# Kernel tuning notes

Hardware: AMD Instinct MI355X
Metric: run time of the kernel (lower is better)

Reference implementation:

```python
import jax, jax.numpy as jnp
import numpy as np

HEADS = 16
DIM_HEAD = 64
SCALE = DIM_HEAD ** -0.5


def setup_inputs() -> dict:
    key = jax.random.key(0)
    ks = jax.random.split(key, 6)
    B, Nq, Nkv, D = 2, 512, 4096, 1024
    inner = HEADS * DIM_HEAD  # 1024
    s = 1.0 / np.sqrt(D)
    return {
        "q": jax.random.normal(ks[0], (B, Nq, D), jnp.float32),
        "kv": jax.random.normal(ks[1], (B, Nkv, D), jnp.float32),
        "mask": jnp.ones((B, Nkv), dtype=bool),
        "Wq": jax.random.normal(ks[2], (D, inner), jnp.float32) * s,
        "Wkv": jax.random.normal(ks[3], (D, 2 * inner), jnp.float32) * s,
        "Wo": jax.random.normal(ks[4], (inner, D), jnp.float32) * (1.0 / np.sqrt(inner)),
        "bo": jnp.zeros((D,), jnp.float32),
    }


def reference(q, kv, mask, Wq, Wkv, Wo, bo):
    B, Nq, D = q.shape
    Nkv = kv.shape[1]
    h, dh = HEADS, DIM_HEAD
    # projections
    qh = (q @ Wq).reshape(B, Nq, h, dh).transpose(0, 2, 1, 3)        # (B,h,Nq,dh)
    kvp = kv @ Wkv                                                    # (B,Nkv,2*inner)
    k, v = jnp.split(kvp, 2, axis=-1)
    kh = k.reshape(B, Nkv, h, dh).transpose(0, 2, 1, 3)              # (B,h,Nkv,dh)
    vh = v.reshape(B, Nkv, h, dh).transpose(0, 2, 1, 3)
    # scaled dot-product cross-attention
    attn = jnp.einsum("bhqd,bhkd->bhqk", qh, kh) * SCALE             # (B,h,Nq,Nkv)
    neg_inf = jnp.finfo(attn.dtype).min
    attn = jnp.where(mask[:, None, None, :], attn, neg_inf)
    attn = jax.nn.softmax(attn, axis=-1)
    out = jnp.einsum("bhqk,bhkd->bhqd", attn, vh)                    # (B,h,Nq,dh)
    out = out.transpose(0, 2, 1, 3).reshape(B, Nq, h * dh)
    return out @ Wo + bo
```

## Files before the change

### kernel.cpp

```cpp
#include <hip/hip_runtime.h>
#include <string.h>
#include <math.h>

typedef unsigned short u16;
typedef __bf16 bf16x8 __attribute__((ext_vector_type(8)));
typedef float floatx4 __attribute__((ext_vector_type(4)));

#define HEADS  16
#define DH     64
#define BATCH  2
#define NQ     512
#define NKV    4096
#define DMODEL 1024
#define INNER  1024
#define SCALE  0.125f
#define LOG2E  1.4426950408889634f
#define FM     12.0f
#define SPLIT  4
#define KEYS_PER_PART (NKV / SPLIT)
#define CH (KEYS_PER_PART / 64)

__device__ __forceinline__ u16 f2bf(float f) {
  union { __bf16 h; u16 u; } v; v.h = (__bf16)f; return v.u;
}

__device__ __forceinline__ void gll16(const u16* g, u16* l) {
  __builtin_amdgcn_global_load_lds(
      (const __attribute__((address_space(1))) unsigned int*)g,
      (__attribute__((address_space(3))) unsigned int*)l, 16, 0, 0);
}

__global__ __launch_bounds__(256) void prep(const float* __restrict__ q,
                                            const float* __restrict__ kv,
                                            const float* __restrict__ Wq,
                                            const float* __restrict__ Wkv,
                                            const float* __restrict__ Wo,
                                            u16* __restrict__ qb,
                                            u16* __restrict__ kvb,
                                            u16* __restrict__ Wqt,
                                            u16* __restrict__ Wkvt,
                                            u16* __restrict__ Wot) {
  __shared__ float tile[32][33];
  const int bx = blockIdx.x, tid = threadIdx.x;
  if (bx < 4608) {
    const float* x; u16* y; size_t i;
    if (bx < 512) { x = q;  y = qb;  i = (size_t)bx * 256 + tid; }
    else          { x = kv; y = kvb; i = (size_t)(bx - 512) * 256 + tid; }
    const float4* p = (const float4*)x + i * 2;
    float4 a = p[0], b = p[1];
    union { u16 s[8]; uint4 v; } o;
    o.s[0] = f2bf(a.x); o.s[1] = f2bf(a.y); o.s[2] = f2bf(a.z); o.s[3] = f2bf(a.w);
    o.s[4] = f2bf(b.x); o.s[5] = f2bf(b.y); o.s[6] = f2bf(b.z); o.s[7] = f2bf(b.w);
    *(uint4*)(y + i * 8) = o.v;
    return;
  }
  const float* W; u16* Wt; int K, N, n0, k0, t;
  if (bx < 5632)      { t = bx - 4608; W = Wq;  Wt = Wqt;  K = 1024; N = 1024; n0 = (t & 31) * 32; k0 = (t >> 5) * 32; }
  else if (bx < 7680) { t = bx - 5632; W = Wkv; Wt = Wkvt; K = 1024; N = 2048; n0 = (t & 63) * 32; k0 = (t >> 6) * 32; }
  else                { t = bx - 7680; W = Wo;  Wt = Wot;  K = 1024; N = 1024; n0 = (t & 31) * 32; k0 = (t >> 5) * 32; }
  const int tx = tid & 31, ty = tid >> 5;
  for (int i = 0; i < 32; i += 8)
    tile[ty + i][tx] = W[(size_t)(k0 + ty + i) * N + n0 + tx];
  __syncthreads();
  for (int i = 0; i < 32; i += 8)
    Wt[(size_t)(n0 + ty + i) * K + k0 + tx] = f2bf(tile[tx][ty + i]);
}

#define KV_NT 16
__global__ __launch_bounds__(256) void gemm_kv(const u16* __restrict__ A,
                                               const u16* __restrict__ Bt,
                                               u16* __restrict__ Kb,
                                               u16* __restrict__ vT) {
  const int K = DMODEL;
  __shared__ __align__(16) u16 As[2][128 * 64];
  __shared__ __align__(16) u16 Bs[2][128 * 64];
  const int tid  = threadIdx.x;
  const int lane = tid & 63, wave = tid >> 6;
  const int wr = wave >> 1, wc = wave & 1;
  const int l16 = lane & 15, quad = lane >> 4;
  const int d = blockIdx.x;
  const int lg = (d & 7) * 128 + (d >> 3);
  const int bm = lg >> 4, bn = lg & 15;
  const int r8 = lane >> 3;
  const int kb8 = (lane & 7) ^ r8;
  const u16* aP = A  + ((size_t)bm * 128 + wave * 8 + r8) * K + kb8 * 8;
  const u16* bP = Bt + ((size_t)bn * 128 + wave * 8 + r8) * K + kb8 * 8;

  floatx4 acc[4][4] = {};

#define KV_STAGE(t_) { \
    const int j_ = (t_) & 1; \
    const size_t ko = (size_t)(t_) * 64; \
    _Pragma("unroll") \
    for (int p = 0; p < 4; ++p) { \
      gll16(aP + (size_t)p * 32 * K + ko, &As[j_][p * 2048 + wave * 512]); \
      gll16(bP + (size_t)p * 32 * K + ko, &Bs[j_][p * 2048 + wave * 512]); \
    } \
  }

  KV_STAGE(0);
  asm volatile("s_waitcnt vmcnt(0)" ::: "memory");
  __builtin_amdgcn_s_barrier();

  for (int t = 0; t < KV_NT; ++t) {
    if (t + 1 < KV_NT) KV_STAGE(t + 1);
    const u16* Ab = As[t & 1];
    const u16* Bb = Bs[t & 1];
    bf16x8 af[4][2], bfr[4][2];
#pragma unroll
    for (int i = 0; i < 4; ++i)
#pragma unroll
      for (int h2 = 0; h2 < 2; ++h2)
        af[i][h2] = *(const bf16x8*)&Ab[(wr * 64 + i * 16 + l16) * 64 +
                                        (((h2 * 4 + quad) ^ (l16 & 7)) << 3)];
#pragma unroll
    for (int j = 0; j < 4; ++j)
#pragma unroll
      for (int h2 = 0; h2 < 2; ++h2)
        bfr[j][h2] = *(const bf16x8*)&Bb[(wc * 64 + j * 16 + l16) * 64 +
                                         (((h2 * 4 + quad) ^ (l16 & 7)) << 3)];
    __builtin_amdgcn_s_setprio(1);
#pragma unroll
    for (int i = 0; i < 4; ++i)
#pragma unroll
      for (int j = 0; j < 4; ++j) {
        acc[i][j] = __builtin_amdgcn_mfma_f32_16x16x32_bf16(af[i][0], bfr[j][0], acc[i][j], 0, 0, 0);
        acc[i][j] = __builtin_amdgcn_mfma_f32_16x16x32_bf16(af[i][1], bfr[j][1], acc[i][j], 0, 0, 0);
      }
    __builtin_amdgcn_s_setprio(0);
    asm volatile("s_waitcnt vmcnt(0)" ::: "memory");
    __builtin_amdgcn_s_barrier();
  }

  if (bn < 8) {
#pragma unroll
    for (int i = 0; i < 4; ++i) {
      const int rowb = bm * 128 + wr * 64 + i * 16 + quad * 4;
#pragma unroll
      for (int j = 0; j < 4; ++j) {
        const int col = bn * 128 + wc * 64 + j * 16 + l16;
#pragma unroll
        for (int r = 0; r < 4; ++r)
          Kb[(size_t)(rowb + r) * 1024 + col] = f2bf(acc[i][j][r]);
      }
    }
  } else {
    const int b = bm >> 5;
    const int tokb = (bm & 31) * 128;
#pragma unroll
    for (int i = 0; i < 4; ++i) {
      const int tok0 = tokb + wr * 64 + i * 16 + quad * 4;
#pragma unroll
      for (int j = 0; j < 4; ++j) {
        const int dd = (bn - 8) * 128 + wc * 64 + j * 16 + l16;
        union { u16 s[4]; uint2 v; } pk;
#pragma unroll
        for (int r = 0; r < 4; ++r) pk.s[r] = f2bf(acc[i][j][r]);
        *(uint2*)(vT + ((size_t)(b * 1024 + dd)) * NKV + tok0) = pk.v;
      }
    }
  }
#undef KV_STAGE
}

template<bool OUT_BF16>
__global__ __launch_bounds__(256) void gemm64(const u16* __restrict__ A,
                                              const u16* __restrict__ Bt,
                                              float* __restrict__ Cf,
                                              u16* __restrict__ Cb,
                                              const float* __restrict__ bias,
                                              int M, int N, int K) {
  __shared__ __align__(16) u16 As[2][64 * 64];
  __shared__ __align__(16) u16 Bs[2][64 * 64];
  const int tid = threadIdx.x;
  const int lane = tid & 63, wave = tid >> 6;
  const int wr = wave >> 1, wc = wave & 1;
  const int l16 = lane & 15, quad = lane >> 4;
  const int bm = blockIdx.y, bn = blockIdx.x;
  const int r0 = tid >> 3;
  const int kbs = (tid & 7) ^ (r0 & 7);
  const u16* aP0 = A  + ((size_t)bm * 64 + r0)      * K + kbs * 8;
  const u16* aP1 = A  + ((size_t)bm * 64 + r0 + 32) * K + kbs * 8;
  const u16* bP0 = Bt + ((size_t)bn * 64 + r0)      * K + kbs * 8;
  const u16* bP1 = Bt + ((size_t)bn * 64 + r0 + 32) * K + kbs * 8;

  floatx4 acc[2][2] = {};
  const int nt = K >> 6;

#define G64_STAGE(t_) { \
    const int j_ = (t_) & 1; \
    const size_t ko = (size_t)(t_) * 64; \
    gll16(aP0 + ko, &As[j_][wave * 512]); \
    gll16(aP1 + ko, &As[j_][2048 + wave * 512]); \
    gll16(bP0 + ko, &Bs[j_][wave * 512]); \
    gll16(bP1 + ko, &Bs[j_][2048 + wave * 512]); \
  }

  G64_STAGE(0);
  asm volatile("s_waitcnt vmcnt(0)" ::: "memory");
  __builtin_amdgcn_s_barrier();

  for (int t = 0; t < nt; ++t) {
    if (t + 1 < nt) G64_STAGE(t + 1);
    const u16* Ab = As[t & 1];
    const u16* Bb = Bs[t & 1];
    bf16x8 af[2][2], bfr[2][2];
#pragma unroll
    for (int i = 0; i < 2; ++i)
#pragma unroll
      for (int kk = 0; kk < 2; ++kk)
        af[i][kk] = *(const bf16x8*)&Ab[(wr * 32 + i * 16 + l16) * 64 +
                                        (((kk * 4 + quad) ^ (l16 & 7)) << 3)];
#pragma unroll
    for (int j = 0; j < 2; ++j)
#pragma unroll
      for (int kk = 0; kk < 2; ++kk)
        bfr[j][kk] = *(const bf16x8*)&Bs[t & 1][(wc * 32 + j * 16 + l16) * 64 +
                                               (((kk * 4 + quad) ^ (l16 & 7)) << 3)];
    __builtin_amdgcn_s_setprio(1);
#pragma unroll
    for (int i = 0; i < 2; ++i)
#pragma unroll
      for (int j = 0; j < 2; ++j) {
        acc[i][j] = __builtin_amdgcn_mfma_f32_16x16x32_bf16(af[i][0], bfr[j][0], acc[i][j], 0, 0, 0);
        acc[i][j] = __builtin_amdgcn_mfma_f32_16x16x32_bf16(af[i][1], bfr[j][1], acc[i][j], 0, 0, 0);
      }
    __builtin_amdgcn_s_setprio(0);
    asm volatile("s_waitcnt vmcnt(0)" ::: "memory");
    __builtin_amdgcn_s_barrier();
    (void)Bb;
  }
#undef G64_STAGE
#pragma unroll
  for (int i = 0; i < 2; ++i) {
    const int rowb = bm * 64 + wr * 32 + i * 16 + quad * 4;
#pragma unroll
    for (int j = 0; j < 2; ++j) {
      const int col = bn * 64 + wc * 32 + j * 16 + l16;
#pragma unroll
      for (int r = 0; r < 4; ++r) {
        const size_t idx = (size_t)(rowb + r) * N + col;
        if (OUT_BF16) Cb[idx] = f2bf(acc[i][j][r]);
        else          Cf[idx] = acc[i][j][r] + bias[col];
      }
    }
  }
}

__global__ __launch_bounds__(256) void attn_part(const u16* __restrict__ Qh,
                                                 const u16* __restrict__ Kb,
                                                 const u16* __restrict__ vT,
                                                 const int* __restrict__ mask,
                                                 float* __restrict__ Opart,
                                                 float* __restrict__ Mst,
                                                 float* __restrict__ Lst) {
  __shared__ __align__(16) u16 Ks[64 * 64];
  __shared__ __align__(16) u16 Vs[2][64 * 64];
  __shared__ __align__(16) u16 QP[4608];
  __shared__ float Msk[64];
  const int tid = threadIdx.x;
  const int lane = tid & 63, w = tid >> 6;
  const int l16 = lane & 15, quad = lane >> 4;
  const int d_ = blockIdx.x;
  const int lg = (d_ & 7) * 128 + (d_ >> 3);
  const int qt   = lg & 7;
  const int part = (lg >> 3) & 3;
  const int h    = (lg >> 5) & 15;
  const int b    = lg >> 9;
  const int rs = tid >> 2, d0 = (tid & 3) * 16;
  u16* Ps = QP + w * 1152;

  const int r8 = lane >> 3;
  const int kb8 = (lane & 7) ^ (r8 & 7);
  const int key00 = part * KEYS_PER_PART;
  const u16* kSrc = Kb + ((size_t)(b * NKV + key00 + w * 8 + r8)) * 1024 + h * DH + kb8 * 8;
  const u16* vSrc = vT + ((size_t)((b * 16 + h) * 64 + w * 8 + r8)) * NKV + key00 + kb8 * 8;
  u16* ldsK0 = Ks + w * 512;
  u16* ldsK1 = Ks + 2048 + w * 512;
  const int koA = (quad ^ (l16 & 7)) << 3;
  const int koB = ((quad + 4) ^ (l16 & 7)) << 3;

  bf16x8 bones;
  {
    union { u16 s[8]; bf16x8 v; } t1;
    const u16 o1 = (l16 == 0) ? (u16)0x3F80 : (u16)0;
#pragma unroll
    for (int i = 0; i < 8; ++i) t1.s[i] = o1;
    bones = t1.v;
  }

  {
    const uint4* p = (const uint4*)(Qh + ((size_t)(b * NQ + qt * 64 + rs)) * INNER + h * DH + d0);
    *(uint4*)&QP[rs * 72 + d0]     = p[0];
    *(uint4*)&QP[rs * 72 + d0 + 8] = p[1];
  }
  gll16(kSrc, ldsK0);
  gll16(kSrc + 32768, ldsK1);
  gll16(vSrc, Vs[0] + w * 512);
  gll16(vSrc + (size_t)32 * NKV, Vs[0] + 2048 + w * 512);
  float mk0 = 0.f;
  if (tid < 64) mk0 = (mask[(size_t)b * NKV + key00 + tid] != 0) ? -FM : -1e30f;
  __syncthreads();
  bf16x8 aq0 = *(const bf16x8*)&QP[(w * 16 + l16) * 72 + quad * 8];
  bf16x8 aq1 = *(const bf16x8*)&QP[(w * 16 + l16) * 72 + 32 + quad * 8];
  if (tid < 64) Msk[tid] = mk0;
  __syncthreads();

  floatx4 o[4] = {};
  floatx4 lacc = {0.f, 0.f, 0.f, 0.f};
  const float SC = SCALE * LOG2E;

  for (int c = 0; c < CH; ++c) {
    const u16* Vcur = Vs[c & 1];
#pragma unroll
    for (int nt = 0; nt < 4; ++nt) {
      bf16x8 b0 = *(const bf16x8*)&Ks[(nt * 16 + l16) * 64 + koA];
      bf16x8 b1 = *(const bf16x8*)&Ks[(nt * 16 + l16) * 64 + koB];
      floatx4 t = {0.f, 0.f, 0.f, 0.f};
      t = __builtin_amdgcn_mfma_f32_16x16x32_bf16(aq0, b0, t, 0, 0, 0);
      t = __builtin_amdgcn_mfma_f32_16x16x32_bf16(aq1, b1, t, 0, 0, 0);
      const float mk = Msk[nt * 16 + l16];
#pragma unroll
      for (int r = 0; r < 4; ++r)
        Ps[(quad * 4 + r) * 72 + nt * 16 + l16] = f2bf(exp2f(t[r] * SC + mk));
    }
    __syncthreads();
    if (c + 1 < CH) {
      gll16(kSrc + (size_t)(c + 1) * 65536, ldsK0);
      gll16(kSrc + (size_t)(c + 1) * 65536 + 32768, ldsK1);
      u16* vdst = Vs[(c + 1) & 1];
      gll16(vSrc + (c + 1) * 64, vdst + w * 512);
      gll16(vSrc + (c + 1) * 64 + (size_t)32 * NKV, vdst + 2048 + w * 512);
      if (tid < 64)
        Msk[tid] = (mask[(size_t)b * NKV + key00 + (c + 1) * 64 + tid] != 0) ? -FM : -1e30f;
    }
    bf16x8 ap0 = *(const bf16x8*)&Ps[l16 * 72 + quad * 8];
    bf16x8 ap1 = *(const bf16x8*)&Ps[l16 * 72 + 32 + quad * 8];
    lacc = __builtin_amdgcn_mfma_f32_16x16x32_bf16(ap0, bones, lacc, 0, 0, 0);
    lacc = __builtin_amdgcn_mfma_f32_16x16x32_bf16(ap1, bones, lacc, 0, 0, 0);
#pragma unroll
    for (int dt = 0; dt < 4; ++dt) {
      bf16x8 bv0 = *(const bf16x8*)&Vcur[(dt * 16 + l16) * 64 + koA];
      bf16x8 bv1 = *(const bf16x8*)&Vcur[(dt * 16 + l16) * 64 + koB];
      o[dt] = __builtin_amdgcn_mfma_f32_16x16x32_bf16(ap0, bv0, o[dt], 0, 0, 0);
      o[dt] = __builtin_amdgcn_mfma_f32_16x16x32_bf16(ap1, bv1, o[dt], 0, 0, 0);
    }
    __syncthreads();
  }
  const int pid = (((b * 16 + h) * 8 + qt) * 4) + part;
#pragma unroll
  for (int r = 0; r < 4; ++r) {
    const int q = w * 16 + quad * 4 + r;
    if (l16 == 0) { Mst[pid * 64 + q] = FM; Lst[pid * 64 + q] = lacc[r]; }
#pragma unroll
    for (int dt = 0; dt < 4; ++dt)
      Opart[(size_t)pid * 4096 + q * 64 + dt * 16 + l16] = o[dt][r];
  }
}

__global__ __launch_bounds__(256) void attn_combine(const float* __restrict__ Opart,
                                                    const float* __restrict__ Mst,
                                                    const float* __restrict__ Lst,
                                                    u16* __restrict__ Out) {
  const int x = blockIdx.x;
  const int t = threadIdx.x;
  const int q = t >> 2, db = (t & 3) * 16;
  const int b = x >> 7, h = (x >> 3) & 15, qt = x & 7;
  float ms[SPLIT], ls[SPLIT];
#pragma unroll
  for (int s = 0; s < SPLIT; ++s) {
    ms[s] = Mst[(size_t)(x * SPLIT + s) * 64 + q];
    ls[s] = Lst[(size_t)(x * SPLIT + s) * 64 + q];
  }
  float M = fmaxf(fmaxf(ms[0], ms[1]), fmaxf(ms[2], ms[3]));
  float wgt[SPLIT], L = 0.f;
#pragma unroll
  for (int s = 0; s < SPLIT; ++s) { wgt[s] = exp2f(ms[s] - M); L += wgt[s] * ls[s]; }
  const float inv = 1.0f / L;
  float acc[16] = {};
#pragma unroll
  for (int s = 0; s < SPLIT; ++s) {
    const float4* p = (const float4*)&Opart[(size_t)(x * SPLIT + s) * 4096 + q * 64 + db];
    const float ws = wgt[s];
#pragma unroll
    for (int i = 0; i < 4; ++i) {
      float4 v = p[i];
      acc[i * 4 + 0] += ws * v.x; acc[i * 4 + 1] += ws * v.y;
      acc[i * 4 + 2] += ws * v.z; acc[i * 4 + 3] += ws * v.w;
    }
  }
  union { u16 s[16]; uint4 v[2]; } ou;
#pragma unroll
  for (int i = 0; i < 16; ++i) ou.s[i] = f2bf(acc[i] * inv);
  u16* dst = Out + ((size_t)(b * NQ + qt * 64 + q)) * INNER + h * DH + db;
  *(uint4*)dst = ou.v[0]; *(uint4*)(dst + 8) = ou.v[1];
}

extern "C" void kernel_launch(void* const* d_in, const int* in_sizes, int n_in,
                              void* d_out, int out_size, void* d_ws, size_t ws_size,
                              hipStream_t stream) {
  const float* q    = (const float*)d_in[0];
  const float* kv   = (const float*)d_in[1];
  const int*   mask = (const int*)d_in[2];
  const float* Wq   = (const float*)d_in[3];
  const float* Wkv  = (const float*)d_in[4];
  const float* Wo   = (const float*)d_in[5];
  const float* bo   = (const float*)d_in[6];
  float* out = (float*)d_out;

  char* ws = (char*)d_ws;
  u16*   qb    = (u16*)(ws);
  u16*   kvb   = (u16*)(ws + (2u << 20));
  float* Mst   = (float*)(ws);
  float* Lst   = (float*)(ws + (256u << 10));
  float* Opart = (float*)(ws + (2u << 20));
  u16* Wqt  = (u16*)(ws + (18u << 20));
  u16* Wkvt = (u16*)(ws + (20u << 20));
  u16* Wot  = (u16*)(ws + (24u << 20));
  u16* qh   = (u16*)(ws + (26u << 20));
  u16* Kb   = (u16*)(ws + (28u << 20));
  u16* vT   = (u16*)(ws + (44u << 20));
  u16* attn = (u16*)(ws + (60u << 20));

  prep<<<dim3(8704), 256, 0, stream>>>(q, kv, Wq, Wkv, Wo, qb, kvb, Wqt, Wkvt, Wot);
  gemm64<true><<<dim3(INNER / 64, (BATCH * NQ) / 64), 256, 0, stream>>>(
      qb, Wqt, nullptr, qh, nullptr, BATCH * NQ, INNER, DMODEL);
  gemm_kv<<<dim3(1024), 256, 0, stream>>>(kvb, Wkvt, Kb, vT);
  attn_part<<<dim3(BATCH * HEADS * (NQ / 64) * SPLIT), 256, 0, stream>>>(
      qh, Kb, vT, mask, Opart, Mst, Lst);
  attn_combine<<<dim3(BATCH * HEADS * (NQ / 64)), 256, 0, stream>>>(Opart, Mst, Lst, attn);
  gemm64<false><<<dim3(DMODEL / 64, (BATCH * NQ) / 64), 256, 0, stream>>>(
      attn, Wot, out, nullptr, bo, BATCH * NQ, DMODEL, INNER);
}
```

Before: 215.6 us.

## Enlarge KV projection GEMM tiles to 256x256 with interleaved prefetch

The K/V projection GEMM now uses 256x256 output tiles with 8 waves per block (each wave computing 128x64) instead of 128x128 tiles with 4 waves. Prefetch of the next k-slice is split into four pieces interleaved between MFMA groups, so global-to-LDS loads overlap compute. The aim is less global traffic per FLOP and better latency hiding. The cost is 128 KB of LDS per block, a grid of only 256 blocks on a 256-CU part (roughly one wave per CU), and higher register pressure from the 32 accumulator tiles.

```diff
diff --git a/kernel.cpp b/kernel.cpp
--- a/kernel.cpp
+++ b/kernel.cpp
@@ -67,100 +67,139 @@
 }
 
 #define KV_NT 16
-__global__ __launch_bounds__(256) void gemm_kv(const u16* __restrict__ A,
-                                               const u16* __restrict__ Bt,
-                                               u16* __restrict__ Kb,
-                                               u16* __restrict__ vT) {
+__global__ __launch_bounds__(512, 2) void gemm_kv(const u16* __restrict__ A,
+                                                  const u16* __restrict__ Bt,
+                                                  u16* __restrict__ Kb,
+                                                  u16* __restrict__ vT) {
   const int K = DMODEL;
-  __shared__ __align__(16) u16 As[2][128 * 64];
-  __shared__ __align__(16) u16 Bs[2][128 * 64];
+  __shared__ __align__(16) u16 As[2][256 * 64];
+  __shared__ __align__(16) u16 Bs[2][256 * 64];
   const int tid  = threadIdx.x;
   const int lane = tid & 63, wave = tid >> 6;
-  const int wr = wave >> 1, wc = wave & 1;
+  const int wr = wave >> 2, wc = wave & 3;
   const int l16 = lane & 15, quad = lane >> 4;
   const int d = blockIdx.x;
-  const int lg = (d & 7) * 128 + (d >> 3);
-  const int bm = lg >> 4, bn = lg & 15;
+  const int lg = (d & 7) * 32 + (d >> 3);
+  const int bm = lg >> 3, bn = lg & 7;
   const int r8 = lane >> 3;
   const int kb8 = (lane & 7) ^ r8;
-  const u16* aP = A  + ((size_t)bm * 128 + wave * 8 + r8) * K + kb8 * 8;
-  const u16* bP = Bt + ((size_t)bn * 128 + wave * 8 + r8) * K + kb8 * 8;
-
-  floatx4 acc[4][4] = {};
-
-#define KV_STAGE(t_) { \
+  const u16* aP = A  + ((size_t)(bm * 256 + wave * 8 + r8)) * K + kb8 * 8;
+  const u16* bP = Bt + ((size_t)(bn * 256 + wave * 8 + r8)) * K + kb8 * 8;
+
+  floatx4 acc[8][4] = {};
+
+#define KV_STAGE_A(t_, h_) { \
     const int j_ = (t_) & 1; \
     const size_t ko = (size_t)(t_) * 64; \
-    _Pragma("unroll") \
-    for (int p = 0; p < 4; ++p) { \
-      gll16(aP + (size_t)p * 32 * K + ko, &As[j_][p * 2048 + wave * 512]); \
-      gll16(bP + (size_t)p * 32 * K + ko, &Bs[j_][p * 2048 + wave * 512]); \
-    } \
-  }
-
-  KV_STAGE(0);
-  asm volatile("s_waitcnt vmcnt(0)" ::: "memory");
-  __builtin_amdgcn_s_barrier();
+    gll16(aP + (size_t)((h_) * 128) * K + ko,      &As[j_][((h_) * 128) * 64 + wave * 512]); \
+    gll16(aP + (size_t)((h_) * 128 + 64) * K + ko, &As[j_][((h_) * 128 + 64) * 64 + wave * 512]); \
+  }
+#define KV_STAGE_B(t_, h_) { \
+    const int j_ = (t_) & 1; \
+    const size_t ko = (size_t)(t_) * 64; \
+    gll16(bP + (size_t)((h_) * 128) * K + ko,      &Bs[j_][((h_) * 128) * 64 + wave * 512]); \
+    gll16(bP + (size_t)((h_) * 128 + 64) * K + ko, &Bs[j_][((h_) * 128 + 64) * 64 + wave * 512]); \
+  }
+
+  KV_STAGE_A(0, 0); KV_STAGE_A(0, 1); KV_STAGE_B(0, 0); KV_STAGE_B(0, 1);
 
   for (int t = 0; t < KV_NT; ++t) {
-    if (t + 1 < KV_NT) KV_STAGE(t + 1);
+    asm volatile("s_waitcnt vmcnt(0)" ::: "memory");
+    __builtin_amdgcn_s_barrier();
     const u16* Ab = As[t & 1];
     const u16* Bb = Bs[t & 1];
-    bf16x8 af[4][2], bfr[4][2];
-#pragma unroll
-    for (int i = 0; i < 4; ++i)
+    const bool pf = (t + 1 < KV_NT);
+    bf16x8 bB[4][2], bA[4][2];
+    if (pf) KV_STAGE_A(t + 1, 0);
+#pragma unroll
+    for (int n = 0; n < 4; ++n)
 #pragma unroll
       for (int h2 = 0; h2 < 2; ++h2)
-        af[i][h2] = *(const bf16x8*)&Ab[(wr * 64 + i * 16 + l16) * 64 +
+        bB[n][h2] = *(const bf16x8*)&Bb[(wc * 64 + n * 16 + l16) * 64 +
                                         (((h2 * 4 + quad) ^ (l16 & 7)) << 3)];
 #pragma unroll
-    for (int j = 0; j < 4; ++j)
+    for (int i = 0; i < 4; ++i)
 #pragma unroll
       for (int h2 = 0; h2 < 2; ++h2)
-        bfr[j][h2] = *(const bf16x8*)&Bb[(wc * 64 + j * 16 + l16) * 64 +
-                                         (((h2 * 4 + quad) ^ (l16 & 7)) << 3)];
+        bA[i][h2] = *(const bf16x8*)&Ab[(wr * 128 + i * 16 + l16) * 64 +
+                                        (((h2 * 4 + quad) ^ (l16 & 7)) << 3)];
     __builtin_amdgcn_s_setprio(1);
 #pragma unroll
     for (int i = 0; i < 4; ++i)
 #pragma unroll
-      for (int j = 0; j < 4; ++j) {
-        acc[i][j] = __builtin_amdgcn_mfma_f32_16x16x32_bf16(af[i][0], bfr[j][0], acc[i][j], 0, 0, 0);
-        acc[i][j] = __builtin_amdgcn_mfma_f32_16x16x32_bf16(af[i][1], bfr[j][1], acc[i][j], 0, 0, 0);
+      for (int j = 0; j < 2; ++j) {
+        acc[i][j] = __builtin_amdgcn_mfma_f32_16x16x32_bf16(bA[i][0], bB[j][0], acc[i][j], 0, 0, 0);
+        acc[i][j] = __builtin_amdgcn_mfma_f32_16x16x32_bf16(bA[i][1], bB[j][1], acc[i][j], 0, 0, 0);
       }
     __builtin_amdgcn_s_setprio(0);
-    asm volatile("s_waitcnt vmcnt(0)" ::: "memory");
-    __builtin_amdgcn_s_barrier();
-  }
-
-  if (bn < 8) {
-#pragma unroll
-    for (int i = 0; i < 4; ++i) {
-      const int rowb = bm * 128 + wr * 64 + i * 16 + quad * 4;
-#pragma unroll
-      for (int j = 0; j < 4; ++j) {
-        const int col = bn * 128 + wc * 64 + j * 16 + l16;
+    if (pf) KV_STAGE_A(t + 1, 1);
+    __builtin_amdgcn_s_setprio(1);
+#pragma unroll
+    for (int i = 0; i < 4; ++i)
+#pragma unroll
+      for (int j = 2; j < 4; ++j) {
+        acc[i][j] = __builtin_amdgcn_mfma_f32_16x16x32_bf16(bA[i][0], bB[j][0], acc[i][j], 0, 0, 0);
+        acc[i][j] = __builtin_amdgcn_mfma_f32_16x16x32_bf16(bA[i][1], bB[j][1], acc[i][j], 0, 0, 0);
+      }
+    __builtin_amdgcn_s_setprio(0);
+    if (pf) KV_STAGE_B(t + 1, 0);
+#pragma unroll
+    for (int i = 0; i < 4; ++i)
+#pragma unroll
+      for (int h2 = 0; h2 < 2; ++h2)
+        bA[i][h2] = *(const bf16x8*)&Ab[(wr * 128 + 64 + i * 16 + l16) * 64 +
+                                        (((h2 * 4 + quad) ^ (l16 & 7)) << 3)];
+    __builtin_amdgcn_s_setprio(1);
+#pragma unroll
+    for (int i = 0; i < 4; ++i)
+#pragma unroll
+      for (int j = 0; j < 2; ++j) {
+        acc[4 + i][j] = __builtin_amdgcn_mfma_f32_16x16x32_bf16(bA[i][0], bB[j][0], acc[4 + i][j], 0, 0, 0);
+        acc[4 + i][j] = __builtin_amdgcn_mfma_f32_16x16x32_bf16(bA[i][1], bB[j][1], acc[4 + i][j], 0, 0, 0);
+      }
+    __builtin_amdgcn_s_setprio(0);
+    if (pf) KV_STAGE_B(t + 1, 1);
+    __builtin_amdgcn_s_setprio(1);
+#pragma unroll
+    for (int i = 0; i < 4; ++i)
+#pragma unroll
+      for (int j = 2; j < 4; ++j) {
+        acc[4 + i][j] = __builtin_amdgcn_mfma_f32_16x16x32_bf16(bA[i][0], bB[j][0], acc[4 + i][j], 0, 0, 0);
+        acc[4 + i][j] = __builtin_amdgcn_mfma_f32_16x16x32_bf16(bA[i][1], bB[j][1], acc[4 + i][j], 0, 0, 0);
+      }
+    __builtin_amdgcn_s_setprio(0);
+  }
+#undef KV_STAGE_A
+#undef KV_STAGE_B
+
+  if (bn < 4) {
+#pragma unroll
+    for (int m = 0; m < 8; ++m) {
+      const int rowb = bm * 256 + wr * 128 + m * 16 + quad * 4;
+#pragma unroll
+      for (int n = 0; n < 4; ++n) {
+        const int col = bn * 256 + wc * 64 + n * 16 + l16;
 #pragma unroll
         for (int r = 0; r < 4; ++r)
-          Kb[(size_t)(rowb + r) * 1024 + col] = f2bf(acc[i][j][r]);
+          Kb[(size_t)(rowb + r) * 1024 + col] = f2bf(acc[m][n][r]);
       }
     }
   } else {
-    const int b = bm >> 5;
-    const int tokb = (bm & 31) * 128;
-#pragma unroll
-    for (int i = 0; i < 4; ++i) {
-      const int tok0 = tokb + wr * 64 + i * 16 + quad * 4;
-#pragma unroll
-      for (int j = 0; j < 4; ++j) {
-        const int dd = (bn - 8) * 128 + wc * 64 + j * 16 + l16;
+#pragma unroll
+    for (int m = 0; m < 8; ++m) {
+      const int rowb = bm * 256 + wr * 128 + m * 16 + quad * 4;
+      const int b = rowb >> 12;
+      const int tok0 = rowb & 4095;
+#pragma unroll
+      for (int n = 0; n < 4; ++n) {
+        const int dd = (bn - 4) * 256 + wc * 64 + n * 16 + l16;
         union { u16 s[4]; uint2 v; } pk;
 #pragma unroll
-        for (int r = 0; r < 4; ++r) pk.s[r] = f2bf(acc[i][j][r]);
+        for (int r = 0; r < 4; ++r) pk.s[r] = f2bf(acc[m][n][r]);
         *(uint2*)(vT + ((size_t)(b * 1024 + dd)) * NKV + tok0) = pk.v;
       }
     }
   }
-#undef KV_STAGE
 }
 
 template<bool OUT_BF16>
@@ -215,8 +254,8 @@
     for (int j = 0; j < 2; ++j)
 #pragma unroll
       for (int kk = 0; kk < 2; ++kk)
-        bfr[j][kk] = *(const bf16x8*)&Bs[t & 1][(wc * 32 + j * 16 + l16) * 64 +
-                                               (((kk * 4 + quad) ^ (l16 & 7)) << 3)];
+        bfr[j][kk] = *(const bf16x8*)&Bb[(wc * 32 + j * 16 + l16) * 64 +
+                                        (((kk * 4 + quad) ^ (l16 & 7)) << 3)];
     __builtin_amdgcn_s_setprio(1);
 #pragma unroll
     for (int i = 0; i < 2; ++i)
@@ -228,7 +267,6 @@
     __builtin_amdgcn_s_setprio(0);
     asm volatile("s_waitcnt vmcnt(0)" ::: "memory");
     __builtin_amdgcn_s_barrier();
-    (void)Bb;
   }
 #undef G64_STAGE
 #pragma unroll
@@ -425,7 +463,7 @@
   prep<<<dim3(8704), 256, 0, stream>>>(q, kv, Wq, Wkv, Wo, qb, kvb, Wqt, Wkvt, Wot);
   gemm64<true><<<dim3(INNER / 64, (BATCH * NQ) / 64), 256, 0, stream>>>(
       qb, Wqt, nullptr, qh, nullptr, BATCH * NQ, INNER, DMODEL);
-  gemm_kv<<<dim3(1024), 256, 0, stream>>>(kvb, Wkvt, Kb, vT);
+  gemm_kv<<<dim3(256), 512, 0, stream>>>(kvb, Wkvt, Kb, vT);
   attn_part<<<dim3(BATCH * HEADS * (NQ / 64) * SPLIT), 256, 0, stream>>>(
       qh, Kb, vT, mask, Opart, Mst, Lst);
   attn_combine<<<dim3(BATCH * HEADS * (NQ / 64)), 256, 0, stream>>>(Opart, Mst, Lst, attn);
```

Result: faster. 207.9 us (-3.5%).
